# Kernel tuning notes

Hardware: AMD Instinct MI355X
Metric: run time of the kernel (lower is better)

Reference implementation:

```python
import jax, jax.numpy as jnp
import numpy as np

N_NODES = 100000
N_EDGES = 3200000
IN_DIM = 128
HID = 32
NUM_CLUSTER = 30
REG = 0.01


def gcn_conv(x, src, dst, W, b, n_nodes):
    # PyG GCNConv: h = D^{-1/2} (A + I) D^{-1/2} (x @ W) + b
    h = x @ W  # [N, out]
    loop = jnp.arange(n_nodes)
    src2 = jnp.concatenate([src, loop])
    dst2 = jnp.concatenate([dst, loop])
    deg = jax.ops.segment_sum(jnp.ones(src2.shape[0], dtype=h.dtype), dst2, num_segments=n_nodes)
    dinv = jnp.where(deg > 0, jax.lax.rsqrt(deg), 0.0)
    norm = dinv[src2] * dinv[dst2]  # [E+N]
    msg = h[src2] * norm[:, None]
    return jax.ops.segment_sum(msg, dst2, num_segments=n_nodes) + b


def setup_inputs() -> dict:
    key = jax.random.key(0)
    k1, k2, k3, k4, k5 = jax.random.split(key, 5)
    x = jax.random.normal(k1, (N_NODES, IN_DIM), dtype=jnp.float32)
    edge_index = jax.random.randint(k2, (2, N_EDGES), 0, N_NODES, dtype=jnp.int64)
    edge_pred = jax.random.uniform(k3, (N_EDGES,), dtype=jnp.float32)
    # Glorot-ish params for the two GCNConv layers
    W1 = jax.random.normal(k4, (IN_DIM, HID), dtype=jnp.float32) / np.sqrt(IN_DIM)
    b1 = jnp.zeros((HID,), dtype=jnp.float32)
    W2 = jax.random.normal(k5, (HID, NUM_CLUSTER), dtype=jnp.float32) / np.sqrt(HID)
    b2 = jnp.zeros((NUM_CLUSTER,), dtype=jnp.float32)
    return {"x": x, "edge_index": edge_index, "edge_pred": edge_pred,
            "W1": W1, "b1": b1, "W2": W2, "b2": b2}


def reference(x, edge_index, edge_pred, W1, b1, W2, b2):
    src, dst = edge_index[0], edge_index[1]
    n = x.shape[0]
    h = jax.nn.relu(gcn_conv(x, src, dst, W1, b1, n))
    # dropout p=0 -> identity
    logits = gcn_conv(h, src, dst, W2, b2, n)
    FX = jax.nn.softmax(logits, axis=-1)  # [N, C]
    FF = jnp.sum(FX[src] * FX[dst], axis=-1)  # [E]
    NFX = jnp.log(1.0 - FX ** 2)  # [N, C]
    preg = -jnp.sum(jnp.log(1.0001 - jnp.exp(jnp.sum(NFX, axis=0))))
    loss = jnp.mean((FF - edge_pred) ** 2) + REG * preg
    return (FX, loss)
```

## Files before the change

kernel.cpp:

```cpp
#include <hip/hip_runtime.h>
#include <hip/hip_bf16.h>
#include <hip/hip_fp8.h>

#define N_NODES 100000
#define N_EDGES 3200000
#define IN_DIM  128
#define HID     32
#define NCLUS   30
#define EDGE_BLOCKS 12500
#define GRP_BLOCKS  12500

#define BUCK_SHIFT 7
#define BUCK_W     128
#define NBUCK      782
#define PB         128
#define EPB        25000
#define SEG_CAP    8192

#define G1A_BLK    780
#define G1A_ROWS   49920
#define G1B_BLK    783

__device__ __forceinline__ float bf2f(__hip_bfloat16 v) { return __bfloat162float(v); }

__device__ __forceinline__ unsigned char enc8(float v) {
  __hip_fp8_e4m3 t(v); return (unsigned char)t.__x;
}
__device__ __forceinline__ float dec8(unsigned b) {
  __hip_fp8_e4m3 t; t.__x = (__hip_fp8_storage_t)b; return (float)t;
}
__device__ __forceinline__ float dot4_fp8(unsigned a, unsigned b) {
  float r = 0.0f;
  #pragma unroll
  for (int k = 0; k < 4; k++)
    r += dec8((a >> (8 * k)) & 0xffu) * dec8((b >> (8 * k)) & 0xffu);
  return r;
}

__device__ __forceinline__ unsigned sc2(unsigned u, float sc) {
  __hip_bfloat16 h0 = *reinterpret_cast<__hip_bfloat16*>(&u);
  unsigned uh = u >> 16;
  __hip_bfloat16 h1 = *reinterpret_cast<__hip_bfloat16*>(&uh);
  __hip_bfloat16 r0 = __float2bfloat16(__bfloat162float(h0) * sc);
  __hip_bfloat16 r1 = __float2bfloat16(__bfloat162float(h1) * sc);
  unsigned a = *reinterpret_cast<unsigned short*>(&r0);
  unsigned b = *reinterpret_cast<unsigned short*>(&r1);
  return a | (b << 16);
}

__device__ __forceinline__ int edge_at(const int* ei, int row, int e, int f) {
  int v = ei[(row * N_EDGES + e) << f];
  return min(max(v, 0), N_NODES - 1);
}

__global__ void k_detect(const unsigned int* ei, int* flag, float* colsum, double* msed) {
  int t = threadIdx.x;
  if (t < 32) colsum[t] = 0.0f;
  if (t == 32) *msed = 0.0;
  if (t == 0) {
    int zeros = 0;
    for (int i = 1; i < 128; i += 2) zeros += (ei[i] == 0u) ? 1 : 0;
    *flag = (zeros >= 48) ? 1 : 0;
  }
}

__global__ void k_zeroall(int* cnt, float* colsum, double* msed) {
  int t = blockIdx.x * blockDim.x + threadIdx.x;
  if (t < N_NODES) cnt[t] = 0;
  if (t < 32) colsum[t] = 0.0f;
  if (t == 32) *msed = 0.0;
}

__device__ __forceinline__ void gemm1_body(int gb, int row_off, const float* x,
                                           const float* W1, __hip_bfloat16* G1) {
  int lane = threadIdx.x & 63;
  int wid  = threadIdx.x >> 6;
  int j = lane & 31;
  int h = lane >> 5;
  float w[64];
  #pragma unroll
  for (int k = 0; k < 64; k++) w[k] = W1[(h * 64 + k) * HID + j];
  int base = row_off + (gb * 4 + wid) * 16;
  #pragma unroll
  for (int p = 0; p < 8; p++) {
    int n0 = base + 2 * p;
    if (n0 >= N_NODES) return;
    int n1 = n0 + 1;
    const float4* xa = (const float4*)(x + (size_t)n0 * IN_DIM + h * 64);
    const float4* xb = (const float4*)(x + (size_t)n1 * IN_DIM + h * 64);
    float accA = 0.0f, accB = 0.0f;
    #pragma unroll
    for (int c = 0; c < 16; c++) {
      float4 a = xa[c];
      float4 b = xb[c];
      accA += a.x * w[4*c] + a.y * w[4*c+1] + a.z * w[4*c+2] + a.w * w[4*c+3];
      accB += b.x * w[4*c] + b.y * w[4*c+1] + b.z * w[4*c+2] + b.w * w[4*c+3];
    }
    accA += __shfl_xor(accA, 32, 64);
    accB += __shfl_xor(accB, 32, 64);
    if (h == 0) G1[n0 * 32 + j] = __float2bfloat16(accA);
    else        G1[n1 * 32 + j] = __float2bfloat16(accB);
  }
}

__global__ void __launch_bounds__(256) k_f1(const int* ei, const int* flag, int* H,
                                            const float* x, const float* W1, __hip_bfloat16* G1) {
  __shared__ int h[NBUCK];
  if (blockIdx.x >= PB) { gemm1_body(blockIdx.x - PB, 0, x, W1, G1); return; }
  int t = threadIdx.x, p = blockIdx.x;
  for (int i = t; i < NBUCK; i += 256) h[i] = 0;
  __syncthreads();
  int f = *flag;
  int base = p * EPB;
  for (int i = t; i < EPB; i += 256) {
    int d = edge_at(ei, 1, base + i, f);
    atomicAdd(&h[d >> BUCK_SHIFT], 1);
  }
  __syncthreads();
  for (int i = t; i < NBUCK; i += 256) H[p * NBUCK + i] = h[i];
}

__global__ void __launch_bounds__(PB) k_hscan(int* H, int* tot) {
  __shared__ int s[PB];
  int b = blockIdx.x, t = threadIdx.x;
  int v = H[t * NBUCK + b];
  s[t] = v; __syncthreads();
  for (int off = 1; off < PB; off <<= 1) {
    int u = (t >= off) ? s[t - off] : 0;
    __syncthreads();
    s[t] += u;
    __syncthreads();
  }
  H[t * NBUCK + b] = s[t] - v;
  if (t == PB - 1) tot[b] = s[t];
}

__global__ void __launch_bounds__(1024) k_bscan(const int* tot, int* bstart) {
  __shared__ int s[1024];
  int t = threadIdx.x;
  int v = (t < NBUCK) ? tot[t] : 0;
  s[t] = v; __syncthreads();
  for (int off = 1; off < 1024; off <<= 1) {
    int u = (t >= off) ? s[t - off] : 0;
    __syncthreads();
    s[t] += u;
    __syncthreads();
  }
  if (t < NBUCK) bstart[t] = s[t] - v;
  if (t == NBUCK - 1) bstart[NBUCK] = s[t];
}

__global__ void __launch_bounds__(256) k_f2(const int* ei, const int* flag, const int* H,
                                            const int* bstart, unsigned* sorted,
                                            const float* x, const float* W1, __hip_bfloat16* G1) {
  __shared__ int cur[NBUCK];
  if (blockIdx.x >= PB) { gemm1_body(blockIdx.x - PB, G1A_ROWS, x, W1, G1); return; }
  int t = threadIdx.x, p = blockIdx.x;
  for (int i = t; i < NBUCK; i += 256) cur[i] = bstart[i] + H[p * NBUCK + i];
  __syncthreads();
  int f = *flag;
  int base = p * EPB;
  for (int i = t; i < EPB; i += 256) {
    int e = base + i;
    int s = edge_at(ei, 0, e, f);
    int d = edge_at(ei, 1, e, f);
    int slot = atomicAdd(&cur[d >> BUCK_SHIFT], 1);
    sorted[slot] = ((unsigned)s << BUCK_SHIFT) | (unsigned)(d & (BUCK_W - 1));
  }
}

__global__ void __launch_bounds__(256) k_pass2(const unsigned* sorted, const int* bstart,
                                               int* cnt, int* cursor, float* dinv, int* csr,
                                               __hip_bfloat16* G1) {
  __shared__ unsigned se[SEG_CAP];
  __shared__ int scnt[BUCK_W], soff[BUCK_W], scur[BUCK_W];
  __shared__ float sdv[BUCK_W];
  int b = blockIdx.x, t = threadIdx.x;
  int s0 = bstart[b], s1 = bstart[b + 1], len = s1 - s0;
  for (int i = t; i < len && i < SEG_CAP; i += 256) se[i] = sorted[s0 + i];
  if (t < BUCK_W) scnt[t] = 0;
  __syncthreads();
  for (int i = t; i < len; i += 256) {
    unsigned u = (i < SEG_CAP) ? se[i] : sorted[s0 + i];
    atomicAdd(&scnt[u & (BUCK_W - 1)], 1);
  }
  __syncthreads();
  int c = (t < BUCK_W) ? scnt[t] : 0;
  if (t < BUCK_W) soff[t] = c;
  __syncthreads();
  for (int off = 1; off < BUCK_W; off <<= 1) {
    int u = 0;
    if (t >= off && t < BUCK_W) u = soff[t - off];
    __syncthreads();
    if (t < BUCK_W) soff[t] += u;
    __syncthreads();
  }
  if (t < BUCK_W) {
    int ex = soff[t] - c;
    int node = (b << BUCK_SHIFT) + t;
    float dv = rsqrtf((float)(c + 1));
    sdv[t] = dv;
    if (node < N_NODES) {
      cnt[node] = c;
      cursor[node] = s0 + ex;
      dinv[node] = dv;
    }
    scur[t] = ex;
  }
  __syncthreads();
  for (int i = t; i < len; i += 256) {
    unsigned u = (i < SEG_CAP) ? se[i] : sorted[s0 + i];
    int dl = u & (BUCK_W - 1);
    int r = atomicAdd(&scur[dl], 1);
    csr[s0 + r] = (int)(u >> BUCK_SHIFT);
  }
  int nbase = b << BUCK_SHIFT;
  int nlim = min(BUCK_W, N_NODES - nbase);
  uint4* Gv = (uint4*)(G1 + (size_t)nbase * 32);
  for (int q = t; q < nlim * 4; q += 256) {
    float sc = sdv[q >> 2];
    uint4 u = Gv[q];
    u.x = sc2(u.x, sc); u.y = sc2(u.y, sc);
    u.z = sc2(u.z, sc); u.w = sc2(u.w, sc);
    Gv[q] = u;
  }
}

__global__ void k_count(const int* ei, const int* flag, int* cnt) {
  int e = blockIdx.x * blockDim.x + threadIdx.x;
  if (e >= N_EDGES) return;
  int f = *flag;
  atomicAdd(&cnt[edge_at(ei, 1, e, f)], 1);
}

__global__ void k_dinv(const int* cnt, float* dinv) {
  int t = blockIdx.x * blockDim.x + threadIdx.x;
  if (t < N_NODES) dinv[t] = rsqrtf((float)(cnt[t] + 1));
}

__global__ void __launch_bounds__(256) k_agg1f(const __hip_bfloat16* G, const int* cursor,
                                               const int* cnt, const int* csr, const float* dinv,
                                               const float* b1, const float* W2,
                                               __hip_bfloat16* G2) {
  int j = threadIdx.x & 31, g = threadIdx.x >> 5;
  int n = blockIdx.x * 8 + g;
  if (n >= N_NODES) return;
  int len = cnt[n];
  int st = cursor[n];
  float dn = dinv[n];
  float acc = bf2f(G[n * 32 + j]);
  int i = 0;
  for (; i + 16 <= len; i += 16) {
    int s[16];
    #pragma unroll
    for (int q = 0; q < 16; q++) s[q] = csr[st + i + q];
    float v[16];
    #pragma unroll
    for (int q = 0; q < 16; q++) v[q] = bf2f(G[s[q] * 32 + j]);
    #pragma unroll
    for (int q = 0; q < 16; q++) acc += v[q];
  }
  for (; i + 4 <= len; i += 4) {
    int s[4];
    #pragma unroll
    for (int q = 0; q < 4; q++) s[q] = csr[st + i + q];
    float v[4];
    #pragma unroll
    for (int q = 0; q < 4; q++) v[q] = bf2f(G[s[q] * 32 + j]);
    #pragma unroll
    for (int q = 0; q < 4; q++) acc += v[q];
  }
  for (; i < len; i++) acc += bf2f(G[csr[st + i] * 32 + j]);
  float h = fmaxf(dn * acc + b1[j], 0.0f);
  float g2 = 0.0f;
  #pragma unroll
  for (int k = 0; k < HID; k++) {
    float wk = (j < NCLUS) ? W2[k * NCLUS + j] : 0.0f;
    g2 += __shfl(h, k, 32) * wk;
  }
  G2[n * 32 + j] = __float2bfloat16((j < NCLUS) ? g2 * dn : 0.0f);
}

__global__ void __launch_bounds__(256) k_agg2c(const __hip_bfloat16* G, const int* cursor,
                                               const int* cnt, const int* csr, const float* dinv,
                                               const float* b2, float* outp, unsigned char* fx8) {
  int j = threadIdx.x & 31, g = threadIdx.x >> 5;
  int n = blockIdx.x * 8 + g;
  if (n >= N_NODES) return;
  int len = cnt[n];
  int st = cursor[n];
  float acc = bf2f(G[n * 32 + j]);
  int i = 0;
  for (; i + 16 <= len; i += 16) {
    int s[16];
    #pragma unroll
    for (int q = 0; q < 16; q++) s[q] = csr[st + i + q];
    float v[16];
    #pragma unroll
    for (int q = 0; q < 16; q++) v[q] = bf2f(G[s[q] * 32 + j]);
    #pragma unroll
    for (int q = 0; q < 16; q++) acc += v[q];
  }
  for (; i + 4 <= len; i += 4) {
    int s[4];
    #pragma unroll
    for (int q = 0; q < 4; q++) s[q] = csr[st + i + q];
    float v[4];
    #pragma unroll
    for (int q = 0; q < 4; q++) v[q] = bf2f(G[s[q] * 32 + j]);
    #pragma unroll
    for (int q = 0; q < 4; q++) acc += v[q];
  }
  for (; i < len; i++) acc += bf2f(G[csr[st + i] * 32 + j]);
  bool act = (j < NCLUS);
  float logit = act ? fminf(fmaxf(dinv[n] * acc + b2[j], -80.0f), 80.0f) : -1e30f;
  float m = logit;
  #pragma unroll
  for (int mask = 16; mask > 0; mask >>= 1) m = fmaxf(m, __shfl_xor(m, mask, 32));
  float ex = act ? __expf(logit - m) : 0.0f;
  float ssum = ex;
  #pragma unroll
  for (int mask = 16; mask > 0; mask >>= 1) ssum += __shfl_xor(ssum, mask, 32);
  float fx = ex / fmaxf(ssum, 1e-30f);
  if (act) outp[n * NCLUS + j] = fx;
  fx8[n * 32 + j] = enc8(act ? fx : 0.0f);
}

__global__ void __launch_bounds__(256) k_gemm1s(const float* x, const float* W1,
                                                const float* dinv, float* G1) {
  __shared__ float Ws[IN_DIM * HID];
  int tid = threadIdx.x;
  for (int i = tid; i < IN_DIM * HID; i += 256) Ws[i] = W1[i];
  __syncthreads();
  int j = tid & 31, r = tid >> 5;
  int n = blockIdx.x * 8 + r;
  if (n >= N_NODES) return;
  const float* xr = x + (size_t)n * IN_DIM;
  float acc = 0.0f;
  #pragma unroll
  for (int k = 0; k < IN_DIM; k++) acc += xr[k] * Ws[k * HID + j];
  G1[n * 32 + j] = acc * dinv[n];
}

__global__ void __launch_bounds__(256) k_gemm2s(const float* h, const float* W2,
                                                const float* dinv, float* G2) {
  __shared__ float Ws[HID * 32];
  int tid = threadIdx.x;
  for (int i = tid; i < HID * 32; i += 256) Ws[i] = 0.0f;
  __syncthreads();
  for (int i = tid; i < HID * NCLUS; i += 256) {
    int k = i / NCLUS, j = i % NCLUS;
    Ws[k * 32 + j] = W2[i];
  }
  __syncthreads();
  int j = tid & 31, r = tid >> 5;
  int n = blockIdx.x * 8 + r;
  if (n >= N_NODES) return;
  const float* hr = h + (size_t)n * 32;
  float acc = 0.0f;
  #pragma unroll
  for (int k = 0; k < HID; k++) acc += hr[k] * Ws[k * 32 + j];
  G2[n * 32 + j] = (j < NCLUS) ? acc * dinv[n] : 0.0f;
}

__global__ void __launch_bounds__(256) k_eagg2(const int* ei, const int* flag,
                                               const float* G, float* D) {
  int j = threadIdx.x & 31, g = threadIdx.x >> 5;
  int f = *flag;
  for (int e = blockIdx.x * 8 + g; e < N_EDGES; e += gridDim.x * 8) {
    int s = edge_at(ei, 0, e, f);
    int d = edge_at(ei, 1, e, f);
    atomicAdd(&D[d * 32 + j], G[s * 32 + j]);
  }
}

__global__ void k_relu2(const float* A, const float* dinv, const float* b1, float* G) {
  int t = blockIdx.x * blockDim.x + threadIdx.x;
  if (t >= N_NODES * 32) return;
  int n = t >> 5, j = t & 31;
  G[t] = fmaxf(dinv[n] * (A[t] + G[t]) + b1[j], 0.0f);
}

__global__ void __launch_bounds__(256) k_softmax2(const float* S, const float* G2, const float* dinv,
                                                  const float* b2, float* outp) {
  int n = blockIdx.x * blockDim.x + threadIdx.x;
  if (n >= N_NODES) return;
  float di = dinv[n];
  float lg[NCLUS];
  float m = -1e30f;
  #pragma unroll
  for (int j = 0; j < NCLUS; j++) {
    float v = di * (S[n * 32 + j] + G2[n * 32 + j]) + b2[j];
    v = fminf(fmaxf(v, -80.0f), 80.0f);
    lg[j] = v; m = fmaxf(m, v);
  }
  float ssum = 0.0f;
  #pragma unroll
  for (int j = 0; j < NCLUS; j++) { lg[j] = __expf(lg[j] - m); ssum += lg[j]; }
  float inv = 1.0f / ssum;
  #pragma unroll
  for (int j = 0; j < NCLUS; j++) outp[n * NCLUS + j] = lg[j] * inv;
}

__global__ void k_fx8(const float* outp, unsigned char* fx8) {
  int t = blockIdx.x * blockDim.x + threadIdx.x;
  if (t >= N_NODES * 32) return;
  int n = t >> 5, j = t & 31;
  fx8[t] = enc8((j < NCLUS) ? outp[n * NCLUS + j] : 0.0f);
}

__global__ void __launch_bounds__(256) k_msef3(const int* ei, const float* ep,
                                               const uint4* fx8, const int* flag,
                                               double* msed) {
  int f = *flag;
  int tid = blockIdx.x * blockDim.x + threadIdx.x;
  float local = 0.0f;
  for (int e = tid; e < N_EDGES; e += gridDim.x * blockDim.x) {
    int s = edge_at(ei, 0, e, f);
    int d = edge_at(ei, 1, e, f);
    const uint4* rs = fx8 + s * 2;
    const uint4* rd = fx8 + d * 2;
    uint4 a0 = rs[0], a1 = rs[1];
    uint4 b0 = rd[0], b1 = rd[1];
    float acc;
    acc  = dot4_fp8(a0.x, b0.x) + dot4_fp8(a0.y, b0.y)
         + dot4_fp8(a0.z, b0.z) + dot4_fp8(a0.w, b0.w);
    acc += dot4_fp8(a1.x, b1.x) + dot4_fp8(a1.y, b1.y)
         + dot4_fp8(a1.z, b1.z) + dot4_fp8(a1.w, b1.w);
    float diff = acc - ep[e];
    local += diff * diff;
  }
  __shared__ float sd[256];
  sd[threadIdx.x] = local; __syncthreads();
  for (int off = 128; off > 0; off >>= 1) {
    if (threadIdx.x < off) sd[threadIdx.x] += sd[threadIdx.x + off];
    __syncthreads();
  }
  if (threadIdx.x == 0) atomicAdd(msed, (double)sd[0]);
}

__global__ void __launch_bounds__(256) k_colsumf(const float* FX, float* colsum) {
  __shared__ float sd[256];
  int tid = threadIdx.x;
  int j = tid & 31, g = tid >> 5;
  float local = 0.0f;
  if (j < NCLUS) {
    for (int n = blockIdx.x * 8 + g; n < N_NODES; n += gridDim.x * 8) {
      float v = FX[n * NCLUS + j];
      local += log1pf(-v * v);
    }
  }
  sd[tid] = local; __syncthreads();
  if (tid < 32) {
    float s = 0.0f;
    #pragma unroll
    for (int gg = 0; gg < 8; gg++) s += sd[tid + 32 * gg];
    if (tid < NCLUS) atomicAdd(&colsum[tid], s);
  }
}

__global__ void k_final(const float* colsum, const double* msed, float* out) {
  int tid = threadIdx.x;
  float v = 0.0f;
  if (tid < NCLUS) v = logf(1.0001f - __expf(colsum[tid]));
  #pragma unroll
  for (int mask = 32; mask > 0; mask >>= 1) v += __shfl_xor(v, mask, 64);
  if (tid == 0) {
    float preg = -v;
    float msev = (float)(*msed / (double)N_EDGES);
    out[(size_t)N_NODES * NCLUS] = msev + 0.01f * preg;
  }
}

extern "C" void kernel_launch(void* const* d_in, const int* in_sizes, int n_in,
                              void* d_out, int out_size, void* d_ws, size_t ws_size,
                              hipStream_t stream) {
  const float* x  = (const float*)d_in[0];
  const int*   ei = (const int*)d_in[1];
  const float* ep = (const float*)d_in[2];
  const float* W1 = (const float*)d_in[3];
  const float* b1 = (const float*)d_in[4];
  const float* W2 = (const float*)d_in[5];
  const float* b2 = (const float*)d_in[6];
  float* out = (float*)d_out;

  char* ws = (char*)d_ws;
  size_t off = 0;
  auto alloc = [&](size_t bytes) { size_t o = off; off += (bytes + 255) & ~(size_t)255; return o; };

  size_t o_hdr  = alloc(1024);
  size_t o_cnt  = alloc((size_t)N_NODES * 4);
  size_t o_dinv = alloc((size_t)N_NODES * 4);
  size_t o_B1   = alloc((size_t)N_NODES * 32 * 4);
  size_t o_B2   = alloc((size_t)N_NODES * 32 * 4);

  int*    flag   = (int*)(ws + o_hdr);
  double* msed   = (double*)(ws + o_hdr + 8);
  float*  colsum = (float*)(ws + o_hdr + 256);
  int*    cnt    = (int*)(ws + o_cnt);
  float*  dinv   = (float*)(ws + o_dinv);
  float*  B1f    = (float*)(ws + o_B1);
  float*  B2f    = (float*)(ws + o_B2);
  __hip_bfloat16* B1b = (__hip_bfloat16*)(ws + o_B1);
  unsigned char*  B2c = (unsigned char*)(ws + o_B2);

  const int nodeBlocks = (N_NODES + 255) / 256;
  const int edgeBlocks = EDGE_BLOCKS;
  const int grpBlocks  = GRP_BLOCKS;
  const int elemBlocks = (N_NODES * 32 + 255) / 256;

  k_detect<<<1, 64, 0, stream>>>((const unsigned int*)ei, flag, colsum, msed);

  size_t o_cursor = alloc((size_t)N_NODES * 4);
  size_t o_csr    = alloc((size_t)N_EDGES * 4);
  bool use_csr = (off <= ws_size);

  const unsigned char* fx8;

  if (use_csr) {
    int* cursor = (int*)(ws + o_cursor);
    int* csr    = (int*)(ws + o_csr);
    int* H      = (int*)(ws + o_B1 + 6400000);
    int* tot    = (int*)(ws + o_B1 + 6400000 + 401408);
    int* bstart = (int*)(ws + o_B1 + 6400000 + 405504);
    unsigned* sorted = (unsigned*)B2c;

    __hip_bfloat16* G1b = B1b;

    k_f1<<<PB + G1A_BLK, 256, 0, stream>>>(ei, flag, H, x, W1, G1b);
    k_hscan<<<NBUCK, PB, 0, stream>>>(H, tot);
    k_bscan<<<1, 1024, 0, stream>>>(tot, bstart);
    k_f2<<<PB + G1B_BLK, 256, 0, stream>>>(ei, flag, H, bstart, sorted, x, W1, G1b);
    k_pass2<<<NBUCK, 256, 0, stream>>>(sorted, bstart, cnt, cursor, dinv, csr, G1b);

    __hip_bfloat16* G2b = (__hip_bfloat16*)(ws + o_B2 + (size_t)N_NODES * 32);
    unsigned char*  fx  = B2c;

    k_agg1f<<<grpBlocks, 256, 0, stream>>>(G1b, cursor, cnt, csr, dinv, b1, W2, G2b);
    k_agg2c<<<grpBlocks, 256, 0, stream>>>(G2b, cursor, cnt, csr, dinv, b2, out, fx);
    fx8 = fx;
  } else {
    k_zeroall<<<nodeBlocks, 256, 0, stream>>>(cnt, colsum, msed);
    k_count<<<edgeBlocks, 256, 0, stream>>>(ei, flag, cnt);
    k_dinv<<<nodeBlocks, 256, 0, stream>>>(cnt, dinv);
    k_gemm1s<<<grpBlocks, 256, 0, stream>>>(x, W1, dinv, B1f);
    hipMemsetAsync(B2f, 0, (size_t)N_NODES * 32 * 4, stream);
    k_eagg2<<<8192, 256, 0, stream>>>(ei, flag, B1f, B2f);
    k_relu2<<<elemBlocks, 256, 0, stream>>>(B2f, dinv, b1, B1f);
    k_gemm2s<<<grpBlocks, 256, 0, stream>>>(B1f, W2, dinv, B2f);
    hipMemsetAsync(B1f, 0, (size_t)N_NODES * 32 * 4, stream);
    k_eagg2<<<8192, 256, 0, stream>>>(ei, flag, B2f, B1f);
    k_softmax2<<<nodeBlocks, 256, 0, stream>>>(B1f, B2f, dinv, b2, out);
    k_fx8<<<elemBlocks, 256, 0, stream>>>(out, (unsigned char*)B1b);
    fx8 = (const unsigned char*)B1b;
  }

  k_msef3<<<4096, 256, 0, stream>>>(ei, ep, (const uint4*)fx8, flag, msed);
  k_colsumf<<<256, 256, 0, stream>>>(out, colsum);
  k_final<<<1, 64, 0, stream>>>(colsum, msed, out);
}
```

Measured before the change: 478.5 us.

## Restructure first-layer GEMM to one row per thread with W1 staged in LDS

The x@W1 projection, co-scheduled with the edge bucketing kernels, now has each thread compute a full 32-wide output row. It reads W1 from shared memory with broadcast float4 loads and writes packed bf16 with 16-byte stores. Previously each wavefront split K across half-waves, held W1 in registers and reduced with shuffles. The GEMM block count drops accordingly. Per-thread strided row reads of x may coalesce poorly, and the 16 KB LDS per block can lower occupancy for the bucketing blocks that share the kernel.

```diff
diff --git a/kernel.cpp b/kernel.cpp
--- a/kernel.cpp
+++ b/kernel.cpp
@@ -17,9 +17,9 @@
 #define EPB        25000
 #define SEG_CAP    8192
 
-#define G1A_BLK    780
+#define G1A_BLK    195
 #define G1A_ROWS   49920
-#define G1B_BLK    783
+#define G1B_BLK    196
 
 __device__ __forceinline__ float bf2f(__hip_bfloat16 v) { return __bfloat162float(v); }
 
@@ -71,43 +71,64 @@
   if (t == 32) *msed = 0.0;
 }
 
-__device__ __forceinline__ void gemm1_body(int gb, int row_off, const float* x,
-                                           const float* W1, __hip_bfloat16* G1) {
-  int lane = threadIdx.x & 63;
-  int wid  = threadIdx.x >> 6;
-  int j = lane & 31;
-  int h = lane >> 5;
-  float w[64];
-  #pragma unroll
-  for (int k = 0; k < 64; k++) w[k] = W1[(h * 64 + k) * HID + j];
-  int base = row_off + (gb * 4 + wid) * 16;
-  #pragma unroll
-  for (int p = 0; p < 8; p++) {
-    int n0 = base + 2 * p;
-    if (n0 >= N_NODES) return;
-    int n1 = n0 + 1;
-    const float4* xa = (const float4*)(x + (size_t)n0 * IN_DIM + h * 64);
-    const float4* xb = (const float4*)(x + (size_t)n1 * IN_DIM + h * 64);
-    float accA = 0.0f, accB = 0.0f;
-    #pragma unroll
-    for (int c = 0; c < 16; c++) {
-      float4 a = xa[c];
-      float4 b = xb[c];
-      accA += a.x * w[4*c] + a.y * w[4*c+1] + a.z * w[4*c+2] + a.w * w[4*c+3];
-      accB += b.x * w[4*c] + b.y * w[4*c+1] + b.z * w[4*c+2] + b.w * w[4*c+3];
+__device__ __forceinline__ void gemm1_rpl(int gb, int row_off, const float* x,
+                                          const float* Wl, __hip_bfloat16* G1) {
+  int n = row_off + gb * 256 + threadIdx.x;
+  if (n >= N_NODES) return;
+  float acc[32];
+  #pragma unroll
+  for (int j = 0; j < 32; j++) acc[j] = 0.0f;
+  const float4* xp = (const float4*)(x + (size_t)n * IN_DIM);
+  #pragma unroll
+  for (int kc = 0; kc < 4; kc++) {
+    float4 xv[8];
+    #pragma unroll
+    for (int q = 0; q < 8; q++) xv[q] = xp[kc * 8 + q];
+    #pragma unroll
+    for (int q = 0; q < 8; q++) {
+      #pragma unroll
+      for (int e = 0; e < 4; e++) {
+        float xk = (e == 0) ? xv[q].x : (e == 1) ? xv[q].y : (e == 2) ? xv[q].z : xv[q].w;
+        const float4* wr = (const float4*)(Wl + (kc * 32 + q * 4 + e) * HID);
+        #pragma unroll
+        for (int jv = 0; jv < 8; jv++) {
+          float4 w4 = wr[jv];
+          acc[4*jv+0] += xk * w4.x;
+          acc[4*jv+1] += xk * w4.y;
+          acc[4*jv+2] += xk * w4.z;
+          acc[4*jv+3] += xk * w4.w;
+        }
+      }
     }
-    accA += __shfl_xor(accA, 32, 64);
-    accB += __shfl_xor(accB, 32, 64);
-    if (h == 0) G1[n0 * 32 + j] = __float2bfloat16(accA);
-    else        G1[n1 * 32 + j] = __float2bfloat16(accB);
-  }
+  }
+  unsigned pk[16];
+  #pragma unroll
+  for (int jp = 0; jp < 16; jp++) {
+    __hip_bfloat16 l0 = __float2bfloat16(acc[2*jp]);
+    __hip_bfloat16 l1 = __float2bfloat16(acc[2*jp+1]);
+    unsigned a = *reinterpret_cast<unsigned short*>(&l0);
+    unsigned b = *reinterpret_cast<unsigned short*>(&l1);
+    pk[jp] = a | (b << 16);
+  }
+  uint4* dst = (uint4*)(G1 + (size_t)n * 32);
+  dst[0] = make_uint4(pk[0], pk[1], pk[2], pk[3]);
+  dst[1] = make_uint4(pk[4], pk[5], pk[6], pk[7]);
+  dst[2] = make_uint4(pk[8], pk[9], pk[10], pk[11]);
+  dst[3] = make_uint4(pk[12], pk[13], pk[14], pk[15]);
 }
 
 __global__ void __launch_bounds__(256) k_f1(const int* ei, const int* flag, int* H,
                                             const float* x, const float* W1, __hip_bfloat16* G1) {
-  __shared__ int h[NBUCK];
-  if (blockIdx.x >= PB) { gemm1_body(blockIdx.x - PB, 0, x, W1, G1); return; }
-  int t = threadIdx.x, p = blockIdx.x;
+  __shared__ float smem[IN_DIM * HID];
+  int t = threadIdx.x;
+  if (blockIdx.x >= PB) {
+    for (int i = t; i < IN_DIM * HID; i += 256) smem[i] = W1[i];
+    __syncthreads();
+    gemm1_rpl(blockIdx.x - PB, 0, x, smem, G1);
+    return;
+  }
+  int* h = (int*)smem;
+  int p = blockIdx.x;
   for (int i = t; i < NBUCK; i += 256) h[i] = 0;
   __syncthreads();
   int f = *flag;
@@ -153,9 +174,16 @@
 __global__ void __launch_bounds__(256) k_f2(const int* ei, const int* flag, const int* H,
                                             const int* bstart, unsigned* sorted,
                                             const float* x, const float* W1, __hip_bfloat16* G1) {
-  __shared__ int cur[NBUCK];
-  if (blockIdx.x >= PB) { gemm1_body(blockIdx.x - PB, G1A_ROWS, x, W1, G1); return; }
-  int t = threadIdx.x, p = blockIdx.x;
+  __shared__ float smem[IN_DIM * HID];
+  int t = threadIdx.x;
+  if (blockIdx.x >= PB) {
+    for (int i = t; i < IN_DIM * HID; i += 256) smem[i] = W1[i];
+    __syncthreads();
+    gemm1_rpl(blockIdx.x - PB, G1A_ROWS, x, smem, G1);
+    return;
+  }
+  int* cur = (int*)smem;
+  int p = blockIdx.x;
   for (int i = t; i < NBUCK; i += 256) cur[i] = bstart[i] + H[p * NBUCK + i];
   __syncthreads();
   int f = *flag;
```

Result: faster. 461.6 us (-3.5%).
